# Optimization experiments

Measured on AMD Instinct MI355X. Metric: run time of the kernel, lower is better.

The kernel has to match this reference:

```python
import jax, jax.numpy as jnp
import numpy as np
from math import sqrt

B, S, E = 1, 2048, 1024
H, D = 16, 1024          # num_heads, d_model
DH = D // H              # head_dim = 64
EPS = 1e-5
LAMBDA_INIT = 0.8


def setup_inputs() -> dict:
    key = jax.random.key(0)
    ks = jax.random.split(key, 16)
    sd = 0.02
    x = jax.random.normal(ks[0], (B, S, E), dtype=jnp.float32)
    # causal mask: True => masked (matches torch masked_fill semantics)
    mask = jnp.triu(jnp.ones((S, S), dtype=bool), k=1)
    # per-head projection params stacked over heads: W [H, DH, E], b [H, DH]
    mk = lambda k: jax.random.normal(k, (H, DH, E), dtype=jnp.float32) * sd
    bk = lambda k: jax.random.normal(k, (H, DH), dtype=jnp.float32) * sd
    return {
        "x": x, "mask": mask,
        "Wq1": mk(ks[1]), "bq1": bk(ks[2]),
        "Wq2": mk(ks[3]), "bq2": bk(ks[4]),
        "Wk1": mk(ks[5]), "bk1": bk(ks[6]),
        "Wk2": mk(ks[7]), "bk2": bk(ks[8]),
        "Wv": mk(ks[9]), "bv": bk(ks[10]),
        "lam": jnp.full((H,), LAMBDA_INIT, dtype=jnp.float32),
        "gn_w": jnp.ones((D,), dtype=jnp.float32),
        "gn_b": jnp.zeros((D,), dtype=jnp.float32),
        "Wo": jax.random.normal(ks[11], (E, D), dtype=jnp.float32) * sd,
        "bo": jax.random.normal(ks[12], (E,), dtype=jnp.float32) * sd,
    }


def reference(x, mask, Wq1, bq1, Wq2, bq2, Wk1, bk1, Wk2, bk2, Wv, bv,
              lam, gn_w, gn_b, Wo, bo):
    scale = 1.0 / sqrt(DH)
    proj = lambda W, b: jnp.einsum('bse,hde->bhsd', x, W) + b[None, :, None, :]
    q1, q2 = proj(Wq1, bq1), proj(Wq2, bq2)
    k1, k2 = proj(Wk1, bk1), proj(Wk2, bk2)
    v = proj(Wv, bv)                                   # [B,H,S,DH]

    neg_inf = jnp.float32(-jnp.inf)
    s1 = jnp.einsum('bhsd,bhtd->bhst', q1, k1) * scale  # [B,H,S,S]
    s2 = jnp.einsum('bhsd,bhtd->bhst', q2, k2) * scale
    s1 = jnp.where(mask, neg_inf, s1)
    s2 = jnp.where(mask, neg_inf, s2)
    w = jax.nn.softmax(s1, axis=-1) - lam[None, :, None, None] * jax.nn.softmax(s2, axis=-1)
    # dropout is identity in eval mode
    out = jnp.einsum('bhst,bhtd->bhsd', w, v)           # [B,H,S,DH]

    # concat heads along feature dim -> [B,S,D]
    cat = out.transpose(0, 2, 1, 3).reshape(B, S, D)
    # GroupNorm over channels with num_groups=H: normalize each (DH, S) group
    xc = cat.transpose(0, 2, 1).reshape(B, H, DH, S)    # [B,H,DH,S]
    mu = xc.mean(axis=(2, 3), keepdims=True)
    var = xc.var(axis=(2, 3), keepdims=True)
    xn = ((xc - mu) * jax.lax.rsqrt(var + EPS)).reshape(B, D, S)
    xn = xn * gn_w[None, :, None] + gn_b[None, :, None]
    xn = xn.transpose(0, 2, 1)                          # [B,S,D]

    return xn @ Wo.T + bo                               # [B,S,E]
```

## Files before the change

### kernel.cpp

```cpp
#include <hip/hip_runtime.h>

#define S_LEN 2048
#define E_DIM 1024
#define NH 16
#define DHD 64
#define DMODEL 1024

typedef unsigned short u16;
typedef __attribute__((ext_vector_type(8))) short bf16x8;
typedef __attribute__((ext_vector_type(4))) float f32x4;

static constexpr float GN_EPS = 1e-5f;
static constexpr float QSCALE_LOG2E = 0.125f * 1.44269504088896340736f;

struct alignas(8) U16x4 { u16 x, y, z, w; };

__device__ __forceinline__ u16 f2bf(float f) {
    union { float f; unsigned u; } v; v.f = f;
    unsigned r = v.u + 0x7fffu + ((v.u >> 16) & 1u);
    return (u16)(r >> 16);
}
__device__ __forceinline__ u16 f2bf_trunc(float f) {
    union { float f; unsigned u; } v; v.f = f;
    return (u16)(v.u >> 16);
}
__device__ __forceinline__ float bf2f(u16 u) {
    union { unsigned u; float f; } v; v.u = ((unsigned)u) << 16; return v.f;
}

__device__ __forceinline__ f32x4 fzero() { f32x4 z = {0.f, 0.f, 0.f, 0.f}; return z; }

__device__ __forceinline__ void async16(const u16* g, u16* l) {
    __builtin_amdgcn_global_load_lds(
        (const __attribute__((address_space(1))) unsigned int*)g,
        (__attribute__((address_space(3))) unsigned int*)l, 16, 0, 0);
}

__device__ __forceinline__ void stage8(const u16* gbase, int gstride, u16* lds,
                                       int r0, int l) {
    const int cg = (l & 7) ^ (l >> 3);
    async16(gbase + (size_t)(r0 + (l >> 3)) * gstride + cg * 8, lds + r0 * 64);
}

__device__ __forceinline__ bf16x8 ldsfrag(const u16* lds, int r, int chunk) {
    return *(const bf16x8*)((const char*)lds + r * 128 + ((chunk ^ (r & 7)) << 4));
}

__global__ __launch_bounds__(256) void f2b_kernel(
    const float* __restrict__ x,
    const float* __restrict__ w0, const float* __restrict__ w1,
    const float* __restrict__ w2, const float* __restrict__ w3,
    const float* __restrict__ w4, const float* __restrict__ wo,
    u16* __restrict__ xb, u16* __restrict__ wall, u16* __restrict__ dwo)
{
    const int z = blockIdx.z;
    const float* src; u16* dst; int n;
    const int nw = NH * DHD * E_DIM;
    switch (z) {
        case 0: src = x;  dst = xb;            n = S_LEN * E_DIM;  break;
        case 1: src = w0; dst = wall;          n = nw; break;
        case 2: src = w1; dst = wall + nw;     n = nw; break;
        case 3: src = w2; dst = wall + 2 * nw; n = nw; break;
        case 4: src = w3; dst = wall + 3 * nw; n = nw; break;
        case 5: src = w4; dst = wall + 4 * nw; n = nw; break;
        default: src = wo; dst = dwo;          n = DMODEL * E_DIM; break;
    }
    int i = blockIdx.x * 256 + threadIdx.x;
    if (i * 4 < n) {
        float4 v = ((const float4*)src)[i];
        U16x4 o;
        o.x = f2bf(v.x); o.y = f2bf(v.y); o.z = f2bf(v.z); o.w = f2bf(v.w);
        ((U16x4*)dst)[i] = o;
    }
}

__global__ __launch_bounds__(256) void proj_mfma_kernel(
    const u16* __restrict__ xb, const u16* __restrict__ wall,
    const float* __restrict__ bq1, const float* __restrict__ bq2,
    const float* __restrict__ bk1, const float* __restrict__ bk2,
    const float* __restrict__ bv,
    u16* __restrict__ qk, u16* __restrict__ vt)
{
    __shared__ u16 As[128 * 64], Bs[128 * 64];
    const int m0 = blockIdx.x * 128, n0 = blockIdx.y * 128;
    const int t = threadIdx.x, w = t >> 6, l = t & 63;
    const int lane15 = l & 15, quad = l >> 4;
    const int wr = (w >> 1) * 64, wc = (w & 1) * 64;

    f32x4 acc[4][4];
    #pragma unroll
    for (int mi = 0; mi < 4; ++mi)
        #pragma unroll
        for (int ni = 0; ni < 4; ++ni) acc[mi][ni] = fzero();

    const u16* Ag = xb + (size_t)m0 * E_DIM;
    const u16* Bg = wall + (size_t)n0 * E_DIM;

    for (int k0 = 0; k0 < E_DIM; k0 += 64) {
        __syncthreads();
        #pragma unroll
        for (int i = 0; i < 4; ++i) stage8(Ag + k0, E_DIM, As, w * 32 + i * 8, l);
        #pragma unroll
        for (int i = 0; i < 4; ++i) stage8(Bg + k0, E_DIM, Bs, w * 32 + i * 8, l);
        __syncthreads();

        bf16x8 a[4][2], b[4][2];
        #pragma unroll
        for (int mi = 0; mi < 4; ++mi) {
            a[mi][0] = ldsfrag(As, wr + mi * 16 + lane15, quad);
            a[mi][1] = ldsfrag(As, wr + mi * 16 + lane15, 4 + quad);
        }
        #pragma unroll
        for (int ni = 0; ni < 4; ++ni) {
            b[ni][0] = ldsfrag(Bs, wc + ni * 16 + lane15, quad);
            b[ni][1] = ldsfrag(Bs, wc + ni * 16 + lane15, 4 + quad);
        }
        #pragma unroll
        for (int mi = 0; mi < 4; ++mi)
            #pragma unroll
            for (int ni = 0; ni < 4; ++ni) {
                acc[mi][ni] = __builtin_amdgcn_mfma_f32_16x16x32_bf16(
                    a[mi][0], b[ni][0], acc[mi][ni], 0, 0, 0);
                acc[mi][ni] = __builtin_amdgcn_mfma_f32_16x16x32_bf16(
                    a[mi][1], b[ni][1], acc[mi][ni], 0, 0, 0);
            }
    }

    const int tid = n0 >> 10;
    const float* bias = (tid == 0) ? bq1 : (tid == 1) ? bq2 :
                        (tid == 2) ? bk1 : (tid == 3) ? bk2 : bv;
    const float scl = (tid <= 1) ? QSCALE_LOG2E : 1.0f;
    const size_t nQKV = (size_t)NH * S_LEN * DHD;

    #pragma unroll
    for (int ni = 0; ni < 4; ++ni) {
        const int n = n0 + wc + ni * 16 + lane15;
        const int h = (n >> 6) & 15, d = n & 63;
        const float bb = bias[n & 1023];
        #pragma unroll
        for (int mi = 0; mi < 4; ++mi) {
            const int m = m0 + wr + mi * 16 + quad * 4;
            if (tid < 4) {
                u16* o = qk + tid * nQKV + ((size_t)h * S_LEN + m) * DHD + d;
                #pragma unroll
                for (int r = 0; r < 4; ++r)
                    o[r * DHD] = f2bf((acc[mi][ni][r] + bb) * scl);
            } else {
                U16x4 pk;
                pk.x = f2bf(acc[mi][ni][0] + bb);
                pk.y = f2bf(acc[mi][ni][1] + bb);
                pk.z = f2bf(acc[mi][ni][2] + bb);
                pk.w = f2bf(acc[mi][ni][3] + bb);
                *(U16x4*)(vt + ((size_t)h * DHD + d) * S_LEN + m) = pk;
            }
        }
    }
}

__global__ __launch_bounds__(256) void attn_mfma_kernel(
    const u16* __restrict__ qbase, const u16* __restrict__ kbase,
    const u16* __restrict__ vtb, u16* __restrict__ obase)
{
    __shared__ u16 Ks[3][64 * 64], Vs[3][64 * 64];
    __shared__ u16 Ps[4][16 * 64];
    const int z = blockIdx.z, h = blockIdx.y, bb = blockIdx.x;
    const size_t per = (size_t)NH * S_LEN * DHD;
    const u16* qg = qbase + z * per + (size_t)h * S_LEN * DHD;
    const u16* kg = kbase + z * per + (size_t)h * S_LEN * DHD;
    const u16* vg = vtb + (size_t)h * DHD * S_LEN;
    u16* og = obase + z * per + (size_t)h * S_LEN * DHD;
    const int t = threadIdx.x, w = t >> 6, l = t & 63;
    const int lane15 = l & 15, quad = l >> 4;
    u16* Pw = Ps[w];

    for (int half = 0; half < 2; ++half) {
        const int qt = half ? (31 - bb) : bb;
        const int q0 = qt * 64;

        const u16* qrow = qg + (size_t)(q0 + w * 16 + lane15) * DHD + quad * 8;
        bf16x8 qa0 = *(const bf16x8*)(qrow);
        bf16x8 qa1 = *(const bf16x8*)(qrow + 32);

        stage8(kg, DHD, Ks[0], w * 16, l);
        stage8(kg, DHD, Ks[0], w * 16 + 8, l);
        stage8(vg, S_LEN, Vs[0], w * 16, l);
        stage8(vg, S_LEN, Vs[0], w * 16 + 8, l);
        if (qt >= 1) {
            stage8(kg + (size_t)64 * DHD, DHD, Ks[1], w * 16, l);
            stage8(kg + (size_t)64 * DHD, DHD, Ks[1], w * 16 + 8, l);
            stage8(vg + 64, S_LEN, Vs[1], w * 16, l);
            stage8(vg + 64, S_LEN, Vs[1], w * 16 + 8, l);
        }

        f32x4 O[4];
        float lsum[4];
        #pragma unroll
        for (int i = 0; i < 4; ++i) { O[i] = fzero(); lsum[i] = 0.f; }

        int cur = 0, pre = 2;
        for (int kt = 0; kt <= qt; ++kt) {
            if (kt < qt) asm volatile("s_waitcnt vmcnt(4)" ::: "memory");
            else         asm volatile("s_waitcnt vmcnt(0)" ::: "memory");
            asm volatile("s_barrier" ::: "memory");
            if (kt + 2 <= qt) {
                const int t2 = (kt + 2) * 64;
                stage8(kg + (size_t)t2 * DHD, DHD, Ks[pre], w * 16, l);
                stage8(kg + (size_t)t2 * DHD, DHD, Ks[pre], w * 16 + 8, l);
                stage8(vg + t2, S_LEN, Vs[pre], w * 16, l);
                stage8(vg + t2, S_LEN, Vs[pre], w * 16 + 8, l);
            }
            const u16* Kc = Ks[cur];
            const u16* Vc = Vs[cur];

            f32x4 sc[4];
            #pragma unroll
            for (int nt = 0; nt < 4; ++nt) {
                sc[nt] = fzero();
                bf16x8 b0 = ldsfrag(Kc, nt * 16 + lane15, quad);
                bf16x8 b1 = ldsfrag(Kc, nt * 16 + lane15, 4 + quad);
                sc[nt] = __builtin_amdgcn_mfma_f32_16x16x32_bf16(qa0, b0, sc[nt], 0, 0, 0);
                sc[nt] = __builtin_amdgcn_mfma_f32_16x16x32_bf16(qa1, b1, sc[nt], 0, 0, 0);
            }

            const bool diag = (kt == qt);
            #pragma unroll
            for (int r = 0; r < 4; ++r) {
                const int lr = quad * 4 + r;
                const int qrl = w * 16 + lr;
                float p0 = __builtin_amdgcn_exp2f(sc[0][r]);
                float p1 = __builtin_amdgcn_exp2f(sc[1][r]);
                float p2 = __builtin_amdgcn_exp2f(sc[2][r]);
                float p3 = __builtin_amdgcn_exp2f(sc[3][r]);
                if (diag) {
                    if (lane15      > qrl) p0 = 0.f;
                    if (16 + lane15 > qrl) p1 = 0.f;
                    if (32 + lane15 > qrl) p2 = 0.f;
                    if (48 + lane15 > qrl) p3 = 0.f;
                }
                lsum[r] += (p0 + p1) + (p2 + p3);
                const int cb = (lane15 & 7) * 2;
                const int ch = lane15 >> 3;
                char* pb = (char*)Pw + lr * 128;
                *(u16*)(pb + (((0 + ch) ^ (lr & 7)) << 4) + cb) = f2bf_trunc(p0);
                *(u16*)(pb + (((2 + ch) ^ (lr & 7)) << 4) + cb) = f2bf_trunc(p1);
                *(u16*)(pb + (((4 + ch) ^ (lr & 7)) << 4) + cb) = f2bf_trunc(p2);
                *(u16*)(pb + (((6 + ch) ^ (lr & 7)) << 4) + cb) = f2bf_trunc(p3);
            }

            bf16x8 pa0 = ldsfrag(Pw, lane15, quad);
            bf16x8 pa1 = ldsfrag(Pw, lane15, 4 + quad);
            #pragma unroll
            for (int nt = 0; nt < 4; ++nt) {
                bf16x8 v0 = ldsfrag(Vc, nt * 16 + lane15, quad);
                bf16x8 v1 = ldsfrag(Vc, nt * 16 + lane15, 4 + quad);
                O[nt] = __builtin_amdgcn_mfma_f32_16x16x32_bf16(pa0, v0, O[nt], 0, 0, 0);
                O[nt] = __builtin_amdgcn_mfma_f32_16x16x32_bf16(pa1, v1, O[nt], 0, 0, 0);
            }
            cur = (cur == 2) ? 0 : cur + 1;
            pre = (pre == 2) ? 0 : pre + 1;
        }

        float inv[4];
        #pragma unroll
        for (int r = 0; r < 4; ++r) {
            float rs = lsum[r];
            rs += __shfl_xor(rs, 1);
            rs += __shfl_xor(rs, 2);
            rs += __shfl_xor(rs, 4);
            rs += __shfl_xor(rs, 8);
            inv[r] = 1.f / rs;
        }
        u16* orow = og + (size_t)(q0 + w * 16 + quad * 4) * DHD;
        #pragma unroll
        for (int nt = 0; nt < 4; ++nt) {
            const int d = nt * 16 + lane15;
            #pragma unroll
            for (int r = 0; r < 4; ++r)
                orow[r * DHD + d] = f2bf(O[nt][r] * inv[r]);
        }
        __syncthreads();
    }
}

__global__ __launch_bounds__(256) void gn_stats_kernel(
    const u16* __restrict__ o1, const u16* __restrict__ o2,
    const float* __restrict__ lam, float* __restrict__ part)
{
    const int h = blockIdx.x, p = blockIdx.y;
    const float vlam = lam[h];
    const int chunk = S_LEN * DHD / 8;
    const size_t base = (size_t)h * (S_LEN * DHD) + (size_t)p * chunk;
    const uint4* a = (const uint4*)(o1 + base);
    const uint4* b = (const uint4*)(o2 + base);
    float s = 0.f, ss = 0.f;
    for (int i = threadIdx.x; i < chunk / 8; i += 256) {
        uint4 av = a[i], bv = b[i];
        const unsigned aw[4] = {av.x, av.y, av.z, av.w};
        const unsigned bw[4] = {bv.x, bv.y, bv.z, bv.w};
        #pragma unroll
        for (int j = 0; j < 4; ++j) {
            union { unsigned u; float f; } lo_a, hi_a, lo_b, hi_b;
            lo_a.u = aw[j] << 16; hi_a.u = aw[j] & 0xffff0000u;
            lo_b.u = bw[j] << 16; hi_b.u = bw[j] & 0xffff0000u;
            float v0 = lo_a.f - vlam * lo_b.f;
            float v1 = hi_a.f - vlam * hi_b.f;
            s += v0 + v1;
            ss += v0 * v0 + v1 * v1;
        }
    }
    #pragma unroll
    for (int d = 1; d < 64; d <<= 1) { s += __shfl_xor(s, d); ss += __shfl_xor(ss, d); }
    __shared__ float red[8];
    const int w = threadIdx.x >> 6;
    if ((threadIdx.x & 63) == 0) { red[2 * w] = s; red[2 * w + 1] = ss; }
    __syncthreads();
    if (threadIdx.x == 0) {
        float S  = (red[0] + red[2]) + (red[4] + red[6]);
        float SS = (red[1] + red[3]) + (red[5] + red[7]);
        part[(blockIdx.x * 8 + p) * 2]     = S;
        part[(blockIdx.x * 8 + p) * 2 + 1] = SS;
    }
}

__global__ __launch_bounds__(256) void gn_apply_kernel(
    const u16* __restrict__ o1, const u16* __restrict__ o2,
    const float* __restrict__ lam, const float* __restrict__ part,
    const float* __restrict__ gw, const float* __restrict__ gb,
    u16* __restrict__ xnb)
{
    const int i4 = (blockIdx.x * 256 + threadIdx.x) * 4;
    const int dh = i4 & 63;
    const int s  = (i4 >> 6) & (S_LEN - 1);
    const int h  = i4 >> 17;
    const int d  = h * DHD + dh;
    float sum = 0.f, ssum = 0.f;
    #pragma unroll
    for (int p = 0; p < 8; ++p) {
        sum  += part[(h * 8 + p) * 2];
        ssum += part[(h * 8 + p) * 2 + 1];
    }
    const float n = (float)(S_LEN * DHD);
    const float mu = sum / n;
    const float rstd = rsqrtf(ssum / n - mu * mu + GN_EPS);
    const float vlam = lam[h];
    U16x4 a = *(const U16x4*)(o1 + i4);
    U16x4 b = *(const U16x4*)(o2 + i4);
    float4 g4 = *(const float4*)(gw + d);
    float4 b4 = *(const float4*)(gb + d);
    U16x4 o;
    o.x = f2bf((bf2f(a.x) - vlam * bf2f(b.x) - mu) * rstd * g4.x + b4.x);
    o.y = f2bf((bf2f(a.y) - vlam * bf2f(b.y) - mu) * rstd * g4.y + b4.y);
    o.z = f2bf((bf2f(a.z) - vlam * bf2f(b.z) - mu) * rstd * g4.z + b4.z);
    o.w = f2bf((bf2f(a.w) - vlam * bf2f(b.w) - mu) * rstd * g4.w + b4.w);
    *(U16x4*)(xnb + (size_t)s * DMODEL + d) = o;
}

__global__ __launch_bounds__(256) void out_mfma_kernel(
    const u16* __restrict__ xnb, const u16* __restrict__ wob,
    const float* __restrict__ bo, float* __restrict__ out)
{
    __shared__ u16 As[64 * 64], Bs[64 * 64];
    const int m0 = blockIdx.x * 64, n0 = blockIdx.y * 64;
    const int t = threadIdx.x, w = t >> 6, l = t & 63;
    const int lane15 = l & 15, quad = l >> 4;
    f32x4 acc[4];
    #pragma unroll
    for (int nt = 0; nt < 4; ++nt) acc[nt] = fzero();

    const u16* Ag = xnb + (size_t)m0 * DMODEL;
    const u16* Bg = wob + (size_t)n0 * DMODEL;
    for (int k0 = 0; k0 < DMODEL; k0 += 64) {
        __syncthreads();
        stage8(Ag + k0, DMODEL, As, w * 16, l);
        stage8(Ag + k0, DMODEL, As, w * 16 + 8, l);
        stage8(Bg + k0, DMODEL, Bs, w * 16, l);
        stage8(Bg + k0, DMODEL, Bs, w * 16 + 8, l);
        __syncthreads();
        bf16x8 a0 = ldsfrag(As, w * 16 + lane15, quad);
        bf16x8 a1 = ldsfrag(As, w * 16 + lane15, 4 + quad);
        #pragma unroll
        for (int nt = 0; nt < 4; ++nt) {
            bf16x8 b0 = ldsfrag(Bs, nt * 16 + lane15, quad);
            bf16x8 b1 = ldsfrag(Bs, nt * 16 + lane15, 4 + quad);
            acc[nt] = __builtin_amdgcn_mfma_f32_16x16x32_bf16(a0, b0, acc[nt], 0, 0, 0);
            acc[nt] = __builtin_amdgcn_mfma_f32_16x16x32_bf16(a1, b1, acc[nt], 0, 0, 0);
        }
    }
    #pragma unroll
    for (int nt = 0; nt < 4; ++nt) {
        const int n = n0 + nt * 16 + lane15;
        const float bb = bo[n];
        #pragma unroll
        for (int r = 0; r < 4; ++r)
            out[(size_t)(m0 + w * 16 + quad * 4 + r) * E_DIM + n] = acc[nt][r] + bb;
    }
}

extern "C" void kernel_launch(void* const* d_in, const int* in_sizes, int n_in,
                              void* d_out, int out_size, void* d_ws, size_t ws_size,
                              hipStream_t stream)
{
    const float* x   = (const float*)d_in[0];
    const float* Wq1 = (const float*)d_in[2];
    const float* bq1 = (const float*)d_in[3];
    const float* Wq2 = (const float*)d_in[4];
    const float* bq2 = (const float*)d_in[5];
    const float* Wk1 = (const float*)d_in[6];
    const float* bk1 = (const float*)d_in[7];
    const float* Wk2 = (const float*)d_in[8];
    const float* bk2 = (const float*)d_in[9];
    const float* Wv  = (const float*)d_in[10];
    const float* bv  = (const float*)d_in[11];
    const float* lam = (const float*)d_in[12];
    const float* gw  = (const float*)d_in[13];
    const float* gb  = (const float*)d_in[14];
    const float* Wo  = (const float*)d_in[15];
    const float* bo  = (const float*)d_in[16];
    float* out = (float*)d_out;

    char* p = (char*)d_ws;
    auto take = [&](size_t bytes) { char* r = p; p += (bytes + 255) & ~(size_t)255; return r; };
    const size_t nQKV = (size_t)NH * S_LEN * DHD;

    u16* xb   = (u16*)take(2 * (size_t)S_LEN * E_DIM);
    u16* wall = (u16*)take(2 * (size_t)5 * NH * DHD * E_DIM);
    u16* wob  = (u16*)take(2 * (size_t)DMODEL * E_DIM);
    u16* qk   = (u16*)take(2 * 4 * nQKV);
    u16* vtb  = (u16*)take(2 * nQKV);
    u16* o1   = (u16*)take(2 * 2 * nQKV);
    u16* xnb  = (u16*)take(2 * (size_t)S_LEN * DMODEL);
    float* part = (float*)take(4 * 256);

    f2b_kernel<<<dim3(2048, 1, 7), 256, 0, stream>>>(
        x, Wq1, Wq2, Wk1, Wk2, Wv, Wo, xb, wall, wob);

    proj_mfma_kernel<<<dim3(16, 40), 256, 0, stream>>>(
        xb, wall, bq1, bq2, bk1, bk2, bv, qk, vtb);

    attn_mfma_kernel<<<dim3(16, NH, 2), 256, 0, stream>>>(
        qk, qk + 2 * nQKV, vtb, o1);

    gn_stats_kernel<<<dim3(NH, 8), 256, 0, stream>>>(o1, o1 + nQKV, lam, part);
    gn_apply_kernel<<<dim3((int)(nQKV / 1024)), 256, 0, stream>>>(
        o1, o1 + nQKV, lam, part, gw, gb, xnb);

    out_mfma_kernel<<<dim3(32, 16), 256, 0, stream>>>(xnb, wob, bo, out);
}
```

Before: 219.5 us.

## Triple-buffer projection GEMM with async LDS loads and vmcnt waits

The QKV projection GEMM switches from a single-buffered 64-wide K tile with two barriers per iteration to a three-stage ring of 32-wide K tiles. Tiles are prefetched two steps ahead via global_load_lds, with explicit s_waitcnt vmcnt and one s_barrier per step. The aim is to overlap global-to-LDS transfers with MFMA work instead of stalling on each load. In exchange it doubles the number of loop iterations and barriers, and correctness depends on the hand-coded vmcnt count and buffer rotation.

```diff
diff --git a/kernel.cpp b/kernel.cpp
--- a/kernel.cpp
+++ b/kernel.cpp
@@ -41,9 +41,18 @@
     const int cg = (l & 7) ^ (l >> 3);
     async16(gbase + (size_t)(r0 + (l >> 3)) * gstride + cg * 8, lds + r0 * 64);
 }
-
 __device__ __forceinline__ bf16x8 ldsfrag(const u16* lds, int r, int chunk) {
     return *(const bf16x8*)((const char*)lds + r * 128 + ((chunk ^ (r & 7)) << 4));
+}
+
+__device__ __forceinline__ void stage32(const u16* gbase, int gstride, u16* lds,
+                                        int r0, int l) {
+    const int row = l >> 2;
+    const int cg = (l & 3) ^ (row & 3);
+    async16(gbase + (size_t)(r0 + row) * gstride + cg * 8, lds + r0 * 32);
+}
+__device__ __forceinline__ bf16x8 ldsfrag32(const u16* lds, int r, int chunk) {
+    return *(const bf16x8*)((const char*)lds + r * 64 + ((chunk ^ (r & 3)) << 4));
 }
 
 __global__ __launch_bounds__(256) void f2b_kernel(
@@ -81,7 +90,7 @@
     const float* __restrict__ bv,
     u16* __restrict__ qk, u16* __restrict__ vt)
 {
-    __shared__ u16 As[128 * 64], Bs[128 * 64];
+    __shared__ u16 As[3][128 * 32], Bs[3][128 * 32];
     const int m0 = blockIdx.x * 128, n0 = blockIdx.y * 128;
     const int t = threadIdx.x, w = t >> 6, l = t & 63;
     const int lane15 = l & 15, quad = l >> 4;
@@ -96,34 +105,41 @@
     const u16* Ag = xb + (size_t)m0 * E_DIM;
     const u16* Bg = wall + (size_t)n0 * E_DIM;
 
-    for (int k0 = 0; k0 < E_DIM; k0 += 64) {
-        __syncthreads();
-        #pragma unroll
-        for (int i = 0; i < 4; ++i) stage8(Ag + k0, E_DIM, As, w * 32 + i * 8, l);
-        #pragma unroll
-        for (int i = 0; i < 4; ++i) stage8(Bg + k0, E_DIM, Bs, w * 32 + i * 8, l);
-        __syncthreads();
-
-        bf16x8 a[4][2], b[4][2];
-        #pragma unroll
-        for (int mi = 0; mi < 4; ++mi) {
-            a[mi][0] = ldsfrag(As, wr + mi * 16 + lane15, quad);
-            a[mi][1] = ldsfrag(As, wr + mi * 16 + lane15, 4 + quad);
-        }
-        #pragma unroll
-        for (int ni = 0; ni < 4; ++ni) {
-            b[ni][0] = ldsfrag(Bs, wc + ni * 16 + lane15, quad);
-            b[ni][1] = ldsfrag(Bs, wc + ni * 16 + lane15, 4 + quad);
-        }
+    auto stageT = [&](int kt, int buf) {
+        const int k0 = kt * 32;
+        stage32(Ag + k0, E_DIM, As[buf], w * 32, l);
+        stage32(Ag + k0, E_DIM, As[buf], w * 32 + 16, l);
+        stage32(Bg + k0, E_DIM, Bs[buf], w * 32, l);
+        stage32(Bg + k0, E_DIM, Bs[buf], w * 32 + 16, l);
+    };
+    stageT(0, 0);
+    stageT(1, 1);
+
+    int cur = 0, pre = 2;
+    for (int kt = 0; kt < 32; ++kt) {
+        if (kt < 31) asm volatile("s_waitcnt vmcnt(4)" ::: "memory");
+        else         asm volatile("s_waitcnt vmcnt(0)" ::: "memory");
+        asm volatile("s_barrier" ::: "memory");
+        if (kt + 2 < 32) stageT(kt + 2, pre);
+        const u16* Ac = As[cur];
+        const u16* Bc = Bs[cur];
+
+        bf16x8 a[4], b[4];
+        #pragma unroll
+        for (int mi = 0; mi < 4; ++mi)
+            a[mi] = ldsfrag32(Ac, wr + mi * 16 + lane15, quad);
+        #pragma unroll
+        for (int ni = 0; ni < 4; ++ni)
+            b[ni] = ldsfrag32(Bc, wc + ni * 16 + lane15, quad);
         #pragma unroll
         for (int mi = 0; mi < 4; ++mi)
             #pragma unroll
-            for (int ni = 0; ni < 4; ++ni) {
+            for (int ni = 0; ni < 4; ++ni)
                 acc[mi][ni] = __builtin_amdgcn_mfma_f32_16x16x32_bf16(
-                    a[mi][0], b[ni][0], acc[mi][ni], 0, 0, 0);
-                acc[mi][ni] = __builtin_amdgcn_mfma_f32_16x16x32_bf16(
-                    a[mi][1], b[ni][1], acc[mi][ni], 0, 0, 0);
-            }
+                    a[mi], b[ni], acc[mi][ni], 0, 0, 0);
+
+        cur = (cur == 2) ? 0 : cur + 1;
+        pre = (pre == 2) ? 0 : pre + 1;
     }
 
     const int tid = n0 >> 10;
```

Result: slower. 228.8 us (+4.2%).

## Double attention query tile to 128 rows with 8 waves sharing K/V stages

Applied to the files above, without the earlier changes.

The attention kernel now processes 128 query rows per block using 8 waves (512 threads) instead of 64 rows with 4 waves, so each staged K/V tile in LDS is reused by twice as many waves. The grid halves in x and each thread issues half as many async loads per stage. The causal mask now applies to the last two key tiles instead of only the diagonal one. The cost is fewer blocks (256 instead of 512) and some wasted work on the fully masked half of the final tiles.

```diff
diff --git a/kernel.cpp b/kernel.cpp
--- a/kernel.cpp
+++ b/kernel.cpp
@@ -41,7 +41,6 @@
     const int cg = (l & 7) ^ (l >> 3);
     async16(gbase + (size_t)(r0 + (l >> 3)) * gstride + cg * 8, lds + r0 * 64);
 }
-
 __device__ __forceinline__ bf16x8 ldsfrag(const u16* lds, int r, int chunk) {
     return *(const bf16x8*)((const char*)lds + r * 128 + ((chunk ^ (r & 7)) << 4));
 }
@@ -157,12 +156,12 @@
     }
 }
 
-__global__ __launch_bounds__(256) void attn_mfma_kernel(
+__global__ __launch_bounds__(512) void attn_mfma_kernel(
     const u16* __restrict__ qbase, const u16* __restrict__ kbase,
     const u16* __restrict__ vtb, u16* __restrict__ obase)
 {
     __shared__ u16 Ks[3][64 * 64], Vs[3][64 * 64];
-    __shared__ u16 Ps[4][16 * 64];
+    __shared__ u16 Ps[8][16 * 64];
     const int z = blockIdx.z, h = blockIdx.y, bb = blockIdx.x;
     const size_t per = (size_t)NH * S_LEN * DHD;
     const u16* qg = qbase + z * per + (size_t)h * S_LEN * DHD;
@@ -174,23 +173,18 @@
     u16* Pw = Ps[w];
 
     for (int half = 0; half < 2; ++half) {
-        const int qt = half ? (31 - bb) : bb;
-        const int q0 = qt * 64;
+        const int qt = half ? (15 - bb) : bb;
+        const int q0 = qt * 128;
+        const int nkt = 2 * qt + 2;
 
         const u16* qrow = qg + (size_t)(q0 + w * 16 + lane15) * DHD + quad * 8;
         bf16x8 qa0 = *(const bf16x8*)(qrow);
         bf16x8 qa1 = *(const bf16x8*)(qrow + 32);
 
-        stage8(kg, DHD, Ks[0], w * 16, l);
-        stage8(kg, DHD, Ks[0], w * 16 + 8, l);
-        stage8(vg, S_LEN, Vs[0], w * 16, l);
-        stage8(vg, S_LEN, Vs[0], w * 16 + 8, l);
-        if (qt >= 1) {
-            stage8(kg + (size_t)64 * DHD, DHD, Ks[1], w * 16, l);
-            stage8(kg + (size_t)64 * DHD, DHD, Ks[1], w * 16 + 8, l);
-            stage8(vg + 64, S_LEN, Vs[1], w * 16, l);
-            stage8(vg + 64, S_LEN, Vs[1], w * 16 + 8, l);
-        }
+        stage8(kg, DHD, Ks[0], w * 8, l);
+        stage8(vg, S_LEN, Vs[0], w * 8, l);
+        stage8(kg + (size_t)64 * DHD, DHD, Ks[1], w * 8, l);
+        stage8(vg + 64, S_LEN, Vs[1], w * 8, l);
 
         f32x4 O[4];
         float lsum[4];
@@ -198,16 +192,14 @@
         for (int i = 0; i < 4; ++i) { O[i] = fzero(); lsum[i] = 0.f; }
 
         int cur = 0, pre = 2;
-        for (int kt = 0; kt <= qt; ++kt) {
-            if (kt < qt) asm volatile("s_waitcnt vmcnt(4)" ::: "memory");
-            else         asm volatile("s_waitcnt vmcnt(0)" ::: "memory");
+        for (int kt = 0; kt < nkt; ++kt) {
+            if (kt + 1 < nkt) asm volatile("s_waitcnt vmcnt(2)" ::: "memory");
+            else              asm volatile("s_waitcnt vmcnt(0)" ::: "memory");
             asm volatile("s_barrier" ::: "memory");
-            if (kt + 2 <= qt) {
+            if (kt + 2 < nkt) {
                 const int t2 = (kt + 2) * 64;
-                stage8(kg + (size_t)t2 * DHD, DHD, Ks[pre], w * 16, l);
-                stage8(kg + (size_t)t2 * DHD, DHD, Ks[pre], w * 16 + 8, l);
-                stage8(vg + t2, S_LEN, Vs[pre], w * 16, l);
-                stage8(vg + t2, S_LEN, Vs[pre], w * 16 + 8, l);
+                stage8(kg + (size_t)t2 * DHD, DHD, Ks[pre], w * 8, l);
+                stage8(vg + t2, S_LEN, Vs[pre], w * 8, l);
             }
             const u16* Kc = Ks[cur];
             const u16* Vc = Vs[cur];
@@ -222,20 +214,21 @@
                 sc[nt] = __builtin_amdgcn_mfma_f32_16x16x32_bf16(qa1, b1, sc[nt], 0, 0, 0);
             }
 
-            const bool diag = (kt == qt);
+            const bool doMask = (kt + 2 >= nkt);
+            const int toff = kt * 64 - q0;
             #pragma unroll
             for (int r = 0; r < 4; ++r) {
                 const int lr = quad * 4 + r;
-                const int qrl = w * 16 + lr;
                 float p0 = __builtin_amdgcn_exp2f(sc[0][r]);
                 float p1 = __builtin_amdgcn_exp2f(sc[1][r]);
                 float p2 = __builtin_amdgcn_exp2f(sc[2][r]);
                 float p3 = __builtin_amdgcn_exp2f(sc[3][r]);
-                if (diag) {
-                    if (lane15      > qrl) p0 = 0.f;
-                    if (16 + lane15 > qrl) p1 = 0.f;
-                    if (32 + lane15 > qrl) p2 = 0.f;
-                    if (48 + lane15 > qrl) p3 = 0.f;
+                if (doMask) {
+                    const int rel = w * 16 + lr - toff;
+                    if (lane15      > rel) p0 = 0.f;
+                    if (16 + lane15 > rel) p1 = 0.f;
+                    if (32 + lane15 > rel) p2 = 0.f;
+                    if (48 + lane15 > rel) p3 = 0.f;
                 }
                 lsum[r] += (p0 + p1) + (p2 + p3);
                 const int cb = (lane15 & 7) * 2;
@@ -437,7 +430,7 @@
     proj_mfma_kernel<<<dim3(16, 40), 256, 0, stream>>>(
         xb, wall, bq1, bq2, bk1, bk2, bv, qk, vtb);
 
-    attn_mfma_kernel<<<dim3(16, NH, 2), 256, 0, stream>>>(
+    attn_mfma_kernel<<<dim3(8, NH, 2), 512, 0, stream>>>(
         qk, qk + 2 * nQKV, vtb, o1);
 
     gn_stats_kernel<<<dim3(NH, 8), 256, 0, stream>>>(o1, o1 + nQKV, lam, part);
```

Measured after the change: 221.1 us. No clear change (+0.7%).
